# Kernel optimization log

Hardware: AMD Instinct MI355X
Metric: run time of the kernel (lower is better)

The kernel has to match this reference:

```python
import jax, jax.numpy as jnp
import numpy as np

H = W = 28
B = 16384


def _make_masks():
    # pixel groups: 4 interleaved checkerboard-like groups over the 28x28 grid
    pg = np.zeros([4, H, W], np.float32)
    pg[0, ::2, ::2] = 1
    pg[1, 1::2, 1::2] = 1
    pg[2, ::2, 1::2] = 1
    pg[3, 1::2, ::2] = 1
    pcg = pg[:, None]  # [4,1,28,28] (dims[0]=1 channel)
    # information mask x = sum of pixel_channel_groups[:x] (cumulative, exclusive)
    info = np.stack([pcg[:x].sum(0) if x > 0 else np.zeros([1, H, W], np.float32)
                     for x in range(4)])  # [4,1,28,28]
    return jnp.asarray(info), jnp.asarray(pcg)


def setup_inputs() -> dict:
    key = jax.random.key(0)
    k1, k2, k3, k4 = jax.random.split(key, 4)
    samples = jax.random.bernoulli(k1, 0.5, (B, 1, H, W)).astype(jnp.float32)
    position = 0.01 * jax.random.normal(k2, (1, H, W), dtype=jnp.float32)
    weights = 0.1 * jax.random.normal(k3, (4, 1, 2, 3, 3), dtype=jnp.float32)
    biases = 0.1 * jax.random.normal(k4, (4, 1), dtype=jnp.float32)
    return {"samples": samples, "position": position,
            "weights": weights, "biases": biases}


def reference(samples, position, weights, biases):
    info, pcg = _make_masks()
    # position layer broadcast to [B,1,H,W]
    pos = jnp.broadcast_to(position[None], samples.shape)

    def branch(w, b, im, pm):
        # masked input || position channel -> [B,2,H,W]
        inp = jnp.concatenate([samples * im, pos], axis=1)
        logits = jax.lax.conv_general_dilated(
            inp, w, window_strides=(1, 1), padding='SAME',
            dimension_numbers=('NCHW', 'OIHW', 'NCHW')) + b[None, :, None, None]
        # Bernoulli(logits).log_prob(x) = x*logits - softplus(logits)
        lp = samples * logits - jax.nn.softplus(logits)
        return jnp.sum(pm * lp)

    totals = jax.vmap(branch)(weights, biases, info, pcg)  # [4]
    return jnp.sum(totals)
```

## Files before the change

kernel.cpp:

```cpp
#include <hip/hip_runtime.h>


#define NGROUPS 4096
#define GRID    2048
#define TRIPS   (NGROUPS / GRID)

__device__ __forceinline__ float sp_fast(float x) {
    return __logf(1.0f + __expf(x));
}

__device__ __forceinline__ float pos_logit(const float* __restrict__ pos,
                                           const float* __restrict__ w,
                                           const float* __restrict__ b,
                                           int x, int h, int ww) {
    float s = b[x];
    #pragma unroll
    for (int ky = 0; ky < 3; ++ky) {
        #pragma unroll
        for (int kx = 0; kx < 3; ++kx) {
            int hh = h + ky - 1, cc = ww + kx - 1;
            float p = (hh >= 0 && hh < 28 && cc >= 0 && cc < 28) ? pos[hh*28 + cc] : 0.0f;
            s = fmaf(w[x*18 + 9 + ky*3 + kx], p, s);
        }
    }
    return s;
}

__global__ void prep_kernel(const float* __restrict__ pos,
                            const float* __restrict__ w,
                            const float* __restrict__ b,
                            float* __restrict__ tbl,
                            float* __restrict__ out) {
    int u = blockIdx.x * blockDim.x + threadIdx.x;
    if (u == 0) out[0] = 0.0f;
    if (!tbl) return;
    int t = u >> 2, x = u & 3;
    int i = t / 14, j = t % 14;
    bool valid = (t < 196);
    if (x == 0) {
        float C0 = 0.f, S0 = 0.f;
        if (valid) { C0 = pos_logit(pos, w, b, 0, 2*i, 2*j); S0 = sp_fast(C0); }
        tbl[t*8 + 0] = C0; tbl[t*8 + 1] = S0;
    } else if (x == 1) {
        tbl[t*8 + 2] = valid ? pos_logit(pos, w, b, 1, 2*i+1, 2*j+1) : 0.f;
        tbl[t*8 + 5] = 0.f;
    } else if (x == 2) {
        tbl[t*8 + 3] = valid ? pos_logit(pos, w, b, 2, 2*i, 2*j+1) : 0.f;
        tbl[t*8 + 6] = 0.f;
    } else {
        tbl[t*8 + 4] = valid ? pos_logit(pos, w, b, 3, 2*i+1, 2*j) : 0.f;
        tbl[t*8 + 7] = 0.f;
    }
}

template <bool USE_WS>
__global__ __launch_bounds__(256, 4)
void main_kernel(const float* __restrict__ samples,
                 const float* __restrict__ w,
                 const float* __restrict__ tbl,
                 const float* __restrict__ pos,
                 const float* __restrict__ b,
                 float* __restrict__ out) {
    __shared__ float planes[4][4 * 256];
    __shared__ float red[4];
    const int tid = threadIdx.x;
    const int wv = tid >> 6, ln = tid & 63;
    float* myP = planes[wv];

    const float w1a = w[18+0], w1b = w[18+2], w1c = w[18+6], w1d = w[18+8];
    const float w2l = w[36+3], w2r = w[36+5], w2u = w[36+1], w2n = w[36+7];
    const float w3u = w[54+1], w3n = w[54+7], w3l = w[54+3], w3r = w[54+5];
    const float w3a = w[54+0], w3b = w[54+2], w3c = w[54+6], w3e = w[54+8];

    float C0[4], S0[4], P1[4], P2[4], P3[4];
    int oq[4]; bool qv[4];
    #pragma unroll
    for (int k = 0; k < 4; ++k) {
        int t = k*64 + ln;
        qv[k] = (t < 196);
        int i = t / 14, j = t - 14*i;
        oq[k] = (i+1)*16 + (j+1);
        if (USE_WS) {
            const float4* t4 = (const float4*)(tbl + t*8);
            float4 lo = t4[0], hi = t4[1];
            C0[k]=lo.x; S0[k]=lo.y; P1[k]=lo.z; P2[k]=lo.w; P3[k]=hi.x;
        } else {
            C0[k]=S0[k]=P1[k]=P2[k]=P3[k]=0.f;
            if (qv[k]) {
                C0[k] = pos_logit(pos, w, b, 0, 2*i, 2*j);
                S0[k] = sp_fast(C0[k]);
                P1[k] = pos_logit(pos, w, b, 1, 2*i+1, 2*j+1);
                P2[k] = pos_logit(pos, w, b, 2, 2*i, 2*j+1);
                P3[k] = pos_logit(pos, w, b, 3, 2*i+1, 2*j);
            }
        }
    }
    int wo[4];
    #pragma unroll
    for (int k = 0; k < 4; ++k) {
        int g = k*64 + ln;
        int r = g / 7, m = g - 7*r;
        wo[k] = ((r & 1) ? 512 : 0) + ((r >> 1) + 1)*16 + 2*m + 1;
    }

    #pragma unroll
    for (int z = 0; z < 16; ++z) ((float*)planes)[z*256 + tid] = 0.0f;
    __syncthreads();

    float s0sum = S0[0] + S0[1] + S0[2] + S0[3];
    float acc = -(float)TRIPS * s0sum;

    for (int trip = 0; trip < TRIPS; ++trip) {
        int img = (blockIdx.x + trip*GRID) * 4 + wv;
        const float4* src = (const float4*)(samples + (size_t)img * 784);
        #pragma unroll
        for (int k = 0; k < 4; ++k) {
            if (k < 3 || ln < 4) {
                float4 v = src[k*64 + ln];
                float* p = myP + wo[k];
                p[0]   = v.x;  p[256] = v.y;
                p[1]   = v.z;  p[257] = v.w;
            }
        }
        __syncthreads();
        #pragma unroll
        for (int k = 0; k < 4; ++k) {
            if (qv[k]) {
                const int o = oq[k];
                float a00 = myP[o],        a01 = myP[o+1];
                float a10 = myP[o+16],     a11 = myP[o+17];
                float bl  = myP[256+o-1],  bij = myP[256+o];
                float bdl = myP[256+o+15], bdn = myP[256+o+16];
                float cij = myP[512+o];
                float dup = myP[768+o-16], dl  = myP[768+o-1], dij = myP[768+o];

                acc = fmaf(a00, C0[k], acc);
                float L1 = P1[k];
                L1 = fmaf(w1a, a00, L1); L1 = fmaf(w1b, a01, L1);
                L1 = fmaf(w1c, a10, L1); L1 = fmaf(w1d, a11, L1);
                acc += fmaf(dij, L1, -sp_fast(L1));
                float L2 = P2[k];
                L2 = fmaf(w2l, a00, L2); L2 = fmaf(w2r, a01, L2);
                L2 = fmaf(w2u, dup, L2); L2 = fmaf(w2n, dij, L2);
                acc += fmaf(bij, L2, -sp_fast(L2));
                float L3 = P3[k];
                L3 = fmaf(w3u, a00, L3); L3 = fmaf(w3n, a10, L3);
                L3 = fmaf(w3l, dl,  L3); L3 = fmaf(w3r, dij, L3);
                L3 = fmaf(w3a, bl,  L3); L3 = fmaf(w3b, bij, L3);
                L3 = fmaf(w3c, bdl, L3); L3 = fmaf(w3e, bdn, L3);
                acc += fmaf(cij, L3, -sp_fast(L3));
            }
        }
        __syncthreads();
    }

    #pragma unroll
    for (int off = 32; off >= 1; off >>= 1)
        acc += __shfl_xor(acc, off, 64);
    if (ln == 0) red[wv] = acc;
    __syncthreads();
    if (tid == 0) atomicAdd(out, red[0] + red[1] + red[2] + red[3]);
}

extern "C" void kernel_launch(void* const* d_in, const int* in_sizes, int n_in,
                              void* d_out, int out_size, void* d_ws, size_t ws_size,
                              hipStream_t stream) {
    const float* samples  = (const float*)d_in[0];
    const float* position = (const float*)d_in[1];
    const float* weights  = (const float*)d_in[2];
    const float* biases   = (const float*)d_in[3];
    float* out = (float*)d_out;

    bool useWs = (d_ws != nullptr) && (ws_size >= 256 * 8 * sizeof(float));
    float* tbl = useWs ? (float*)d_ws : nullptr;

    prep_kernel<<<4, 256, 0, stream>>>(position, weights, biases, tbl, out);
    if (useWs)
        main_kernel<true ><<<GRID, 256, 0, stream>>>(samples, weights, tbl, position, biases, out);
    else
        main_kernel<false><<<GRID, 256, 0, stream>>>(samples, weights, nullptr, position, biases, out);
}
```

Baseline: 114.7 us.

## Give each wave two contiguous images, drop block barriers, reduce via partials kernel

Each wavefront now owns two consecutive images and loads all four float4 vectors into registers before scattering them to its private shared-memory planes. Because each plane is wave-private, the block-wide __syncthreads are replaced by wave barriers. The per-block atomicAdd is replaced by per-wave partial sums written to workspace and summed in a new single-block final kernel, which costs one extra launch. The fallback path for running without a workspace is removed, so the code now assumes a workspace is always provided.

```diff
diff --git a/kernel.cpp b/kernel.cpp
--- a/kernel.cpp
+++ b/kernel.cpp
@@ -1,9 +1,7 @@
 #include <hip/hip_runtime.h>
 
 
-#define NGROUPS 4096
-#define GRID    2048
-#define TRIPS   (NGROUPS / GRID)
+#define GRID 2048
 
 __device__ __forceinline__ float sp_fast(float x) {
     return __logf(1.0f + __expf(x));
@@ -29,11 +27,8 @@
 __global__ void prep_kernel(const float* __restrict__ pos,
                             const float* __restrict__ w,
                             const float* __restrict__ b,
-                            float* __restrict__ tbl,
-                            float* __restrict__ out) {
+                            float* __restrict__ tbl) {
     int u = blockIdx.x * blockDim.x + threadIdx.x;
-    if (u == 0) out[0] = 0.0f;
-    if (!tbl) return;
     int t = u >> 2, x = u & 3;
     int i = t / 14, j = t % 14;
     bool valid = (t < 196);
@@ -45,7 +40,7 @@
         tbl[t*8 + 2] = valid ? pos_logit(pos, w, b, 1, 2*i+1, 2*j+1) : 0.f;
         tbl[t*8 + 5] = 0.f;
     } else if (x == 2) {
-        tbl[t*8 + 3] = valid ? pos_logit(pos, w, b, 2, 2*i, 2*j+1) : 0.f;
+        tbl[t*8 + 3] = valid ? pos_logit(pos, w, b, 2, 2*i,   2*j+1) : 0.f;
         tbl[t*8 + 6] = 0.f;
     } else {
         tbl[t*8 + 4] = valid ? pos_logit(pos, w, b, 3, 2*i+1, 2*j) : 0.f;
@@ -53,16 +48,12 @@
     }
 }
 
-template <bool USE_WS>
 __global__ __launch_bounds__(256, 4)
 void main_kernel(const float* __restrict__ samples,
                  const float* __restrict__ w,
                  const float* __restrict__ tbl,
-                 const float* __restrict__ pos,
-                 const float* __restrict__ b,
-                 float* __restrict__ out) {
-    __shared__ float planes[4][4 * 256];
-    __shared__ float red[4];
+                 float* __restrict__ partial) {
+    __shared__ float planes[4][1024];
     const int tid = threadIdx.x;
     const int wv = tid >> 6, ln = tid & 63;
     float* myP = planes[wv];
@@ -72,57 +63,44 @@
     const float w3u = w[54+1], w3n = w[54+7], w3l = w[54+3], w3r = w[54+5];
     const float w3a = w[54+0], w3b = w[54+2], w3c = w[54+6], w3e = w[54+8];
 
-    float C0[4], S0[4], P1[4], P2[4], P3[4];
-    int oq[4]; bool qv[4];
+    float C0[4], P1[4], P2[4], P3[4], S0s = 0.f;
+    int oq[4], wo[4]; bool qv[4];
     #pragma unroll
     for (int k = 0; k < 4; ++k) {
         int t = k*64 + ln;
         qv[k] = (t < 196);
         int i = t / 14, j = t - 14*i;
         oq[k] = (i+1)*16 + (j+1);
-        if (USE_WS) {
-            const float4* t4 = (const float4*)(tbl + t*8);
-            float4 lo = t4[0], hi = t4[1];
-            C0[k]=lo.x; S0[k]=lo.y; P1[k]=lo.z; P2[k]=lo.w; P3[k]=hi.x;
-        } else {
-            C0[k]=S0[k]=P1[k]=P2[k]=P3[k]=0.f;
-            if (qv[k]) {
-                C0[k] = pos_logit(pos, w, b, 0, 2*i, 2*j);
-                S0[k] = sp_fast(C0[k]);
-                P1[k] = pos_logit(pos, w, b, 1, 2*i+1, 2*j+1);
-                P2[k] = pos_logit(pos, w, b, 2, 2*i, 2*j+1);
-                P3[k] = pos_logit(pos, w, b, 3, 2*i+1, 2*j);
-            }
-        }
-    }
-    int wo[4];
-    #pragma unroll
-    for (int k = 0; k < 4; ++k) {
-        int g = k*64 + ln;
-        int r = g / 7, m = g - 7*r;
+        const float4* t4 = (const float4*)(tbl + t*8);
+        float4 lo = t4[0], hi = t4[1];
+        C0[k] = lo.x; S0s += lo.y; P1[k] = lo.z; P2[k] = lo.w; P3[k] = hi.x;
+        int r = t / 7, m = t - 7*r;
         wo[k] = ((r & 1) ? 512 : 0) + ((r >> 1) + 1)*16 + 2*m + 1;
     }
 
     #pragma unroll
-    for (int z = 0; z < 16; ++z) ((float*)planes)[z*256 + tid] = 0.0f;
-    __syncthreads();
+    for (int z = 0; z < 4; ++z)
+        ((float4*)myP)[z*64 + ln] = float4{0.f, 0.f, 0.f, 0.f};
 
-    float s0sum = S0[0] + S0[1] + S0[2] + S0[3];
-    float acc = -(float)TRIPS * s0sum;
+    float acc = -2.0f * S0s;
+    const int img0 = blockIdx.x * 8 + wv * 2;
 
-    for (int trip = 0; trip < TRIPS; ++trip) {
-        int img = (blockIdx.x + trip*GRID) * 4 + wv;
-        const float4* src = (const float4*)(samples + (size_t)img * 784);
+    #pragma unroll
+    for (int im = 0; im < 2; ++im) {
+        const float4* src = (const float4*)(samples + (size_t)(img0 + im) * 784);
+        float4 v[4];
         #pragma unroll
-        for (int k = 0; k < 4; ++k) {
+        for (int k = 0; k < 4; ++k)
+            if (k < 3 || ln < 4) v[k] = src[k*64 + ln];
+        __builtin_amdgcn_wave_barrier();
+        #pragma unroll
+        for (int k = 0; k < 4; ++k)
             if (k < 3 || ln < 4) {
-                float4 v = src[k*64 + ln];
                 float* p = myP + wo[k];
-                p[0]   = v.x;  p[256] = v.y;
-                p[1]   = v.z;  p[257] = v.w;
+                p[0]   = v[k].x;  p[256] = v[k].y;
+                p[1]   = v[k].z;  p[257] = v[k].w;
             }
-        }
-        __syncthreads();
+        __builtin_amdgcn_wave_barrier();
         #pragma unroll
         for (int k = 0; k < 4; ++k) {
             if (qv[k]) {
@@ -151,15 +129,26 @@
                 acc += fmaf(cij, L3, -sp_fast(L3));
             }
         }
-        __syncthreads();
     }
 
     #pragma unroll
     for (int off = 32; off >= 1; off >>= 1)
         acc += __shfl_xor(acc, off, 64);
-    if (ln == 0) red[wv] = acc;
+    if (ln == 0) partial[blockIdx.x * 4 + wv] = acc;
+}
+
+__global__ void final_kernel(const float* __restrict__ partial,
+                             float* __restrict__ out) {
+    __shared__ float red[4];
+    const int tid = threadIdx.x;
+    float s = 0.f;
+    #pragma unroll
+    for (int i = 0; i < 32; ++i) s += partial[i*256 + tid];
+    #pragma unroll
+    for (int off = 32; off >= 1; off >>= 1) s += __shfl_xor(s, off, 64);
+    if ((tid & 63) == 0) red[tid >> 6] = s;
     __syncthreads();
-    if (tid == 0) atomicAdd(out, red[0] + red[1] + red[2] + red[3]);
+    if (tid == 0) out[0] = red[0] + red[1] + red[2] + red[3];
 }
 
 extern "C" void kernel_launch(void* const* d_in, const int* in_sizes, int n_in,
@@ -169,14 +158,12 @@
     const float* position = (const float*)d_in[1];
     const float* weights  = (const float*)d_in[2];
     const float* biases   = (const float*)d_in[3];
+    float* ws_f = (float*)d_ws;
+    float* tbl     = ws_f;
+    float* partial = ws_f + 2048;
     float* out = (float*)d_out;
 
-    bool useWs = (d_ws != nullptr) && (ws_size >= 256 * 8 * sizeof(float));
-    float* tbl = useWs ? (float*)d_ws : nullptr;
-
-    prep_kernel<<<4, 256, 0, stream>>>(position, weights, biases, tbl, out);
-    if (useWs)
-        main_kernel<true ><<<GRID, 256, 0, stream>>>(samples, weights, tbl, position, biases, out);
-    else
-        main_kernel<false><<<GRID, 256, 0, stream>>>(samples, weights, nullptr, position, biases, out);
+    prep_kernel<<<4, 256, 0, stream>>>(position, weights, biases, tbl);
+    main_kernel<<<GRID, 256, 0, stream>>>(samples, weights, tbl, partial);
+    final_kernel<<<1, 256, 0, stream>>>(partial, out);
 }
```

After: 95.50 us, median of 2. 16.8% less time.
